# Performance work log

Hardware: AMD Instinct MI355X
Metric: run time of the kernel (lower is better)

## Reference

```python
import jax, jax.numpy as jnp
from jax import lax
import numpy as np

B, L, M, D, K, STRIDE = 32, 32768, 32, 128, 16, 8


def setup_inputs() -> dict:
    key = jax.random.key(0)
    k1, k2, k3, k4 = jax.random.split(key, 4)
    x = jax.random.normal(k1, (B, L, M), dtype=jnp.float32)
    # sorted timestamps per sample, like torch.sort(rand*100)
    timestamps = jnp.sort(jax.random.uniform(k2, (B, L), dtype=jnp.float32) * 100.0, axis=1)
    fan_in = M * K
    bound = 1.0 / np.sqrt(fan_in)
    conv_w = jax.random.uniform(k3, (D, M, K), dtype=jnp.float32, minval=-bound, maxval=bound)
    conv_b = jax.random.uniform(k4, (D,), dtype=jnp.float32, minval=-bound, maxval=bound)
    return {"x": x, "timestamps": timestamps, "conv_w": conv_w, "conv_b": conv_b}


def reference(x, timestamps, conv_w, conv_b):
    # Conv1d patch embedding: x [B,L,M] -> NCL -> conv -> [B,P,D]
    patches = lax.conv_general_dilated(
        x.transpose(0, 2, 1), conv_w,
        window_strides=(STRIDE,), padding=[(0, 0)],
        dimension_numbers=("NCH", "OIH", "NCH"))
    patches = patches.transpose(0, 2, 1) + conv_b  # [B,P,D]
    P = patches.shape[1]

    # Per-patch median timestamp (padding=0 -> all windows full length K).
    # torch.median on even-length returns the LOWER median = sorted idx (K-1)//2.
    starts = jnp.arange(P) * STRIDE
    idx = starts[:, None] + jnp.arange(K)          # [P,K]
    windows = timestamps[:, idx]                   # [B,P,K]
    med = jnp.sort(windows, axis=-1)[..., (K - 1) // 2]  # [B,P]

    # Sinusoidal PE at continuous times.
    div_term = jnp.exp(jnp.arange(0, D, 2).astype(jnp.float32) * (-np.log(10000.0) / D))
    ang = med[..., None] * div_term                # [B,P,D//2]
    pe = jnp.stack([jnp.sin(ang), jnp.cos(ang)], axis=-1).reshape(med.shape[0], P, D)
    return patches + pe
```

## Files before the change

### kernel.cpp

```cpp
#include <hip/hip_runtime.h>
#include <hip/hip_bf16.h>

#define Bn 32
#define Ln 32768
#define Mn 32
#define Dn 128
#define Pn 4095

typedef short  bf16x8 __attribute__((ext_vector_type(8)));
typedef float  f32x4  __attribute__((ext_vector_type(4)));

union BU { bf16x8 v; unsigned short u[8]; };

static __device__ __forceinline__ unsigned short f2bf(float f) {
  __hip_bfloat16 h = __float2bfloat16(f);
  return *reinterpret_cast<unsigned short*>(&h);
}

static __device__ __forceinline__ void gload_lds16(const float* g, float* l) {
  __builtin_amdgcn_global_load_lds(
      (const __attribute__((address_space(1))) unsigned int*)g,
      (__attribute__((address_space(3))) unsigned int*)l, 16, 0, 0);
}

__global__ __launch_bounds__(256) void prep_w_kernel(const float* __restrict__ w,
                                                     unsigned short* __restrict__ wswz) {
  int idx = blockIdx.x * 256 + threadIdx.x;
  int j = idx & 7;
  int d = (idx >> 3) & 127;
  int g = idx >> 10;
  int kk = g * 8 + j;
  int k = kk >> 5;
  int m = kk & 31;
  wswz[idx] = f2bf(w[(d << 9) + (m << 4) + k]);
}

#define QROWS 136
#define BATCHF 288
#define BUFF (16 * BATCHF + 256)

__global__ __launch_bounds__(512, 4) void gemm_pe_kernel(
    const float* __restrict__ x,
    const float* __restrict__ ts,
    const unsigned short* __restrict__ wswz,
    const float* __restrict__ bias,
    float* __restrict__ out) {

  __shared__ float xsf[2][BUFF];
  __shared__ float tsl[256];

  const int b    = blockIdx.y;
  const int pt   = blockIdx.x;
  const int tid  = threadIdx.x;
  const int lane = tid & 63;
  const int wv   = tid >> 6;
  const int mrow = lane & 15;
  const int quad = lane >> 4;

  const float* xb0 = x + (size_t)b * Ln * Mn;

  const int d0 = wv * 16 + mrow;
  const unsigned short* bbase = wswz + (((quad << 7) + d0) << 3);
  bf16x8 bw[16];
  #pragma unroll
  for (int t = 0; t < 16; ++t)
    bw[t] = *reinterpret_cast<const bf16x8*>(bbase + t * 4096);

  if (tid < 256) tsl[tid] = ts[(size_t)b * Ln + (size_t)(pt * 256 + tid) * 8 + 7];

  const float NEG_C = -0.14391156831212810f;
  const float div0  = __expf(NEG_C * (float)(d0 >> 1));
  const float phs   = (d0 & 1) ? 1.5707963267948966f : 0.0f;
  const float bias0 = bias[d0];

#define STAGE(qq, bf)                                                          \
  do {                                                                         \
    const float* gq = xb0 + (size_t)(pt * 2048 + (qq) * 128) * 32;             \
    _Pragma("unroll")                                                          \
    for (int i = 0; i < 2; ++i) {                                              \
      const int bb = wv * 2 + i;                                               \
      gload_lds16(gq + (size_t)bb * 256 + lane * 4,                            \
                  &xsf[bf][bb * BATCHF + (bb & 7) * 4]);                       \
    }                                                                          \
    if (wv == 0 && pt * 2048 + (qq) * 128 + QROWS <= Ln)                       \
      gload_lds16(gq + 4096 + lane * 4, &xsf[bf][16 * BATCHF]);                \
  } while (0)

  STAGE(0, 0);
  __syncthreads();

  #pragma unroll 1
  for (int q = 0; q < 16; ++q) {
    if (q < 15) STAGE(q + 1, (q + 1) & 1);
    __builtin_amdgcn_sched_barrier(0);

    const float* xbuf = xsf[q & 1];
    f32x4 acc = {0.f, 0.f, 0.f, 0.f};
    #pragma unroll
    for (int t = 0; t < 16; ++t) {
      const int b0 = mrow + (t >> 3);
      const int fo = b0 * BATCHF + ((b0 & 7) + (t & 7) * 8 + quad * 2) * 4;
      f32x4 af0 = *reinterpret_cast<const f32x4*>(&xbuf[fo]);
      f32x4 af1 = *reinterpret_cast<const f32x4*>(&xbuf[fo + 4]);
      BU bu;
      bu.u[0] = f2bf(af0[0]); bu.u[1] = f2bf(af0[1]);
      bu.u[2] = f2bf(af0[2]); bu.u[3] = f2bf(af0[3]);
      bu.u[4] = f2bf(af1[0]); bu.u[5] = f2bf(af1[1]);
      bu.u[6] = f2bf(af1[2]); bu.u[7] = f2bf(af1[3]);
      acc = __builtin_amdgcn_mfma_f32_16x16x32_bf16(bu.v, bw[t], acc, 0, 0, 0);
    }

    {
      const int plb = quad * 4;
      f32x4 med4 = *reinterpret_cast<const f32x4*>(&tsl[q * 16 + plb]);
      const int pg = pt * 256 + q * 16 + plb;
      float* obase = out + ((size_t)b * Pn + pg) * Dn + d0;
      #pragma unroll
      for (int reg = 0; reg < 4; ++reg) {
        if (pg + reg < Pn) {
          float m = med4[reg];
          obase[reg * Dn] = acc[reg] + bias0 + __sinf(m * div0 + phs);
        }
      }
    }

    __syncthreads();
  }
#undef STAGE
}

extern "C" void kernel_launch(void* const* d_in, const int* in_sizes, int n_in,
                              void* d_out, int out_size, void* d_ws, size_t ws_size,
                              hipStream_t stream) {
  const float* x      = (const float*)d_in[0];
  const float* ts     = (const float*)d_in[1];
  const float* conv_w = (const float*)d_in[2];
  const float* conv_b = (const float*)d_in[3];
  float* out = (float*)d_out;
  unsigned short* wswz = (unsigned short*)d_ws;

  prep_w_kernel<<<256, 256, 0, stream>>>(conv_w, wswz);
  gemm_pe_kernel<<<dim3(16, Bn), 512, 0, stream>>>(x, ts, wswz, conv_b, out);
}
```

Baseline: 225.7 us.

## Triple-buffer x staging with two-ahead prefetch and partial vmcnt waits

Moves from double to triple LDS buffering so the kernel prefetches two quarters ahead. Full __syncthreads are replaced with explicit s_waitcnt vmcnt counts and raw barriers, so only the oldest stage is waited on while newer loads stay in flight. The tail-row load is made unconditional so every wave issues a fixed number of loads per stage, which keeps the counts correct. In exchange LDS use grows by about 19KB per block, which may cut occupancy below the 4 blocks per CU the launch bounds request. The hand-written wait counts also depend on the compiler not adding other outstanding vector-memory loads or stores.

```diff
diff --git a/kernel.cpp b/kernel.cpp
--- a/kernel.cpp
+++ b/kernel.cpp
@@ -46,7 +46,7 @@
     const float* __restrict__ bias,
     float* __restrict__ out) {
 
-  __shared__ float xsf[2][BUFF];
+  __shared__ float xsf[3][BUFF];
   __shared__ float tsl[256];
 
   const int b    = blockIdx.y;
@@ -82,19 +82,30 @@
       gload_lds16(gq + (size_t)bb * 256 + lane * 4,                            \
                   &xsf[bf][bb * BATCHF + (bb & 7) * 4]);                       \
     }                                                                          \
-    if (wv == 0 && pt * 2048 + (qq) * 128 + QROWS <= Ln)                       \
-      gload_lds16(gq + 4096 + lane * 4, &xsf[bf][16 * BATCHF]);                \
+    if (wv == 0) {                                                             \
+      const float* gt = (pt * 2048 + (qq) * 128 + QROWS <= Ln) ? gq + 4096     \
+                                                               : gq;          \
+      gload_lds16(gt + lane * 4, &xsf[bf][16 * BATCHF]);                       \
+    }                                                                          \
   } while (0)
 
   STAGE(0, 0);
-  __syncthreads();
+  STAGE(1, 1);
+  if (wv == 0) asm volatile("s_waitcnt vmcnt(3) lgkmcnt(0)" ::: "memory");
+  else         asm volatile("s_waitcnt vmcnt(2) lgkmcnt(0)" ::: "memory");
+  __builtin_amdgcn_s_barrier();
+  __builtin_amdgcn_sched_barrier(0);
 
+  int rb = 0;
   #pragma unroll 1
   for (int q = 0; q < 16; ++q) {
-    if (q < 15) STAGE(q + 1, (q + 1) & 1);
+    if (q < 14) {
+      int sb = rb + 2; if (sb >= 3) sb -= 3;
+      STAGE(q + 2, sb);
+    }
     __builtin_amdgcn_sched_barrier(0);
 
-    const float* xbuf = xsf[q & 1];
+    const float* xbuf = xsf[rb];
     f32x4 acc = {0.f, 0.f, 0.f, 0.f};
     #pragma unroll
     for (int t = 0; t < 16; ++t) {
@@ -108,6 +119,15 @@
       bu.u[4] = f2bf(af1[0]); bu.u[5] = f2bf(af1[1]);
       bu.u[6] = f2bf(af1[2]); bu.u[7] = f2bf(af1[3]);
       acc = __builtin_amdgcn_mfma_f32_16x16x32_bf16(bu.v, bw[t], acc, 0, 0, 0);
+    }
+
+    if (q < 15) {
+      if (q < 14) {
+        if (wv == 0) asm volatile("s_waitcnt vmcnt(3)" ::: "memory");
+        else         asm volatile("s_waitcnt vmcnt(2)" ::: "memory");
+      } else {
+        asm volatile("s_waitcnt vmcnt(0)" ::: "memory");
+      }
     }
 
     {
@@ -124,7 +144,11 @@
       }
     }
 
-    __syncthreads();
+    if (q < 15) {
+      __builtin_amdgcn_s_barrier();
+      __builtin_amdgcn_sched_barrier(0);
+    }
+    rb = (rb == 2) ? 0 : rb + 1;
   }
 #undef STAGE
 }
```

Measured after the change: 226.4 us. Within noise of the previous version (+0.3%).
